# Optimization experiments

Hardware: AMD Instinct MI355X
Metric: run time of the kernel (lower is better)

Reference implementation:

```python
import jax, jax.numpy as jnp
import numpy as np

N = 4096      # sentences in document
K = 32        # clusters (args.k)
D = 256       # input_dim
H = 128       # hidden_dim
P_SAL = 0.5   # args.percent_sal


def setup_inputs() -> dict:
    key = jax.random.key(0)
    ks = jax.random.split(key, 12)
    s = 1.0 / np.sqrt(H)
    inp = {
        "sent_gae_embeds": jax.random.normal(ks[0], (N, D), jnp.float32),
        "labels": jax.random.randint(ks[1], (N,), 0, K),
        # GRU layer 0 (torch gate order r,z,n)
        "W_ih0": jax.random.uniform(ks[2], (3 * H, D), jnp.float32, -s, s),
        "W_hh0": jax.random.uniform(ks[3], (3 * H, H), jnp.float32, -s, s),
        "b_ih0": jax.random.uniform(ks[4], (3 * H,), jnp.float32, -s, s),
        "b_hh0": jax.random.uniform(ks[5], (3 * H,), jnp.float32, -s, s),
        # GRU layer 1
        "W_ih1": jax.random.uniform(ks[6], (3 * H, H), jnp.float32, -s, s),
        "W_hh1": jax.random.uniform(ks[7], (3 * H, H), jnp.float32, -s, s),
        "b_ih1": jax.random.uniform(ks[8], (3 * H,), jnp.float32, -s, s),
        "b_hh1": jax.random.uniform(ks[9], (3 * H,), jnp.float32, -s, s),
        # weight-normed linear: W = g * v / ||v|| (norm over input dim)
        "lin_v": jax.random.normal(ks[10], (1, D + H), jnp.float32) * 0.05,
        "lin_g": jnp.ones((1, 1), jnp.float32),
        "lin_b": jnp.zeros((1,), jnp.float32),
    }
    return inp


def _gru_layer(x, W_ih, W_hh, b_ih, b_hh):
    # x: [T, B, Din] -> outputs [T, B, H]
    xw = jnp.einsum("tbd,gd->tbg", x, W_ih) + b_ih  # precompute input gates

    def step(h, xw_t):
        hw = h @ W_hh.T + b_hh
        r = jax.nn.sigmoid(xw_t[:, :H] + hw[:, :H])
        z = jax.nn.sigmoid(xw_t[:, H:2 * H] + hw[:, H:2 * H])
        n = jnp.tanh(xw_t[:, 2 * H:] + r * hw[:, 2 * H:])
        h_new = (1.0 - z) * n + z * h
        return h_new, h_new

    h0 = jnp.zeros((x.shape[1], H), x.dtype)
    _, outs = jax.lax.scan(step, h0, xw)
    return outs


def reference(sent_gae_embeds, labels, W_ih0, W_hh0, b_ih0, b_hh0,
              W_ih1, W_hh1, b_ih1, b_hh1, lin_v, lin_g, lin_b):
    # --- cluster gather: position of each sentence within its cluster ---
    onehot = jax.nn.one_hot(labels, K, dtype=jnp.int32)          # [N, K]
    pos = jnp.cumsum(onehot, axis=0)[jnp.arange(N), labels] - 1  # [N]
    lengths = onehot.sum(axis=0)                                 # [K]

    # padded per-cluster sequences: [T=N, B=K, D]
    padded = jnp.zeros((N, K, D), sent_gae_embeds.dtype).at[pos, labels].set(sent_gae_embeds)

    # --- 2-layer GRU over each cluster sequence ---
    h1 = _gru_layer(padded, W_ih0, W_hh0, b_ih0, b_hh0)
    h2 = _gru_layer(h1, W_ih1, W_hh1, b_ih1, b_hh1)
    len_c = jnp.maximum(lengths, 1)  # empty cluster -> length-1 zero sequence
    cluster_embeds = h2[len_c - 1, jnp.arange(K)]  # [K, H]

    # --- scatter cluster embeds back onto sentences (sent detached as in torch) ---
    sent_d = jax.lax.stop_gradient(sent_gae_embeds)
    final_embeds = jnp.concatenate([sent_d, cluster_embeds[labels]], axis=-1)  # [N, D+H]

    # weight-normed linear + tanh
    Wn = lin_g * lin_v / jnp.linalg.norm(lin_v, axis=1, keepdims=True)
    scores = jnp.tanh(final_embeds @ Wn.T + lin_b)[:, 0]  # [N]

    # salience: per-cluster segment-sum normalization
    clu_scores = jax.ops.segment_sum(scores, labels, num_segments=K)
    sal_scores = scores / clu_scores[labels]

    # position scores: max(0.5, exp(-(i+1)/n**(1/3)))
    inv = np.float32(1.0 / (N ** (1.0 / 3.0)))
    pos_scores = jnp.maximum(0.5, jnp.exp(-(jnp.arange(N, dtype=jnp.float32) + 1.0) * inv))

    return P_SAL * sal_scores + (1.0 - P_SAL) * pos_scores
```

## Files before the change

kernel.cpp:

```cpp
#include <hip/hip_runtime.h>
#include <cmath>

#define NN 4096
#define KK 32
#define DD 256
#define HH 128
#define G3 384
#define CH 16
#define RH 136

typedef __attribute__((ext_vector_type(8))) _Float16 h8;
typedef __attribute__((ext_vector_type(4))) float f32x4;

__global__ __launch_bounds__(256) void prep_k(
    const int* __restrict__ labels, const float* __restrict__ lin_v,
    const float* __restrict__ lin_g,
    const float* __restrict__ Whh0, const float* __restrict__ Wih1,
    const float* __restrict__ Whh1,
    const float* __restrict__ sent, const float* __restrict__ W_ih0,
    const float* __restrict__ b_ih0,
    int* __restrict__ order, int* __restrict__ len, float* __restrict__ scale,
    _Float16* __restrict__ P, float* __restrict__ xw) {
  const int blk = blockIdx.x;
  const int t = threadIdx.x;
  if (blk < 72) {
    const int gid = blk * 256 + t;
    const int lane = gid & 63;
    const int kt = (gid >> 6) & 3;
    const int nt = (gid >> 8) % 24;
    const int mat = (gid >> 8) / 24;
    const float* W = (mat == 0) ? Whh0 : (mat == 1 ? Wih1 : Whh1);
    const int n = nt * 16 + (lane & 15);
    const int kbase = kt * 32 + (lane >> 4) * 8;
    _Float16* dst = P + (size_t)gid * 8;
#pragma unroll
    for (int j = 0; j < 8; ++j) dst[j] = (_Float16)W[(size_t)n * HH + kbase + j];
    return;
  }
  if (blk < 80) {
    const int wv = t >> 6, lane = t & 63;
    const int c = (blk - 72) * 4 + wv;
    int count = 0;
    for (int base = 0; base < NN; base += 64) {
      const int i = base + lane;
      const bool f = (labels[i] == c);
      const unsigned long long m = __ballot(f);
      if (f) order[c * NN + count + __popcll(m & ((1ull << lane) - 1ull))] = i;
      count += __popcll(m);
    }
    if (lane == 0) len[c] = count;
    return;
  }
  if (blk == 80) {
    if (t < 64) {
      float s = 0.f;
      for (int j = t; j < G3; j += 64) { const float v = lin_v[j]; s += v * v; }
      for (int off = 32; off; off >>= 1) s += __shfl_down(s, off);
      if (t == 0) scale[0] = lin_g[0] / sqrtf(s);
    }
    return;
  }
  __shared__ float Xs[16][132];
  __shared__ float Ws[16][68];
  const int g = blk - 81;
  const int i0 = (g & 31) * 128;
  const int g0 = (g >> 5) * 64;
  const int it = t & 15;
  const int gt = t >> 4;
  float acc[8][4] = {};
  for (int k0 = 0; k0 < DD; k0 += 16) {
#pragma unroll
    for (int l = 0; l < 2; ++l) {
      const int u = t * 2 + l;
      const int r = u >> 2;
      const int cq = u & 3;
      const float4 f = *(const float4*)(sent + (size_t)(i0 + r) * DD + k0 + cq * 4);
      Xs[cq * 4 + 0][r] = f.x; Xs[cq * 4 + 1][r] = f.y;
      Xs[cq * 4 + 2][r] = f.z; Xs[cq * 4 + 3][r] = f.w;
    }
    {
      const int r = t >> 2;
      const int cq = t & 3;
      const float4 f = *(const float4*)(W_ih0 + (size_t)(g0 + r) * DD + k0 + cq * 4);
      Ws[cq * 4 + 0][r] = f.x; Ws[cq * 4 + 1][r] = f.y;
      Ws[cq * 4 + 2][r] = f.z; Ws[cq * 4 + 3][r] = f.w;
    }
    __syncthreads();
#pragma unroll
    for (int k = 0; k < 16; ++k) {
      float a[8], b[4];
#pragma unroll
      for (int x = 0; x < 8; ++x) a[x] = Xs[k][it * 8 + x];
#pragma unroll
      for (int y = 0; y < 4; ++y) b[y] = Ws[k][gt * 4 + y];
#pragma unroll
      for (int x = 0; x < 8; ++x)
#pragma unroll
        for (int y = 0; y < 4; ++y)
          acc[x][y] += a[x] * b[y];
    }
    __syncthreads();
  }
  const float4 bs = *(const float4*)(b_ih0 + g0 + gt * 4);
#pragma unroll
  for (int x = 0; x < 8; ++x) {
    const int gi = i0 + it * 8 + x;
    float4 o;
    o.x = acc[x][0] + bs.x; o.y = acc[x][1] + bs.y;
    o.z = acc[x][2] + bs.z; o.w = acc[x][3] + bs.w;
    *(float4*)(xw + (size_t)gi * G3 + g0 + gt * 4) = o;
  }
}

__global__ __launch_bounds__(768) void gru_fused_k(
    const float* __restrict__ xw0,
    const _Float16* __restrict__ pack,
    const float* __restrict__ b_hh0, const float* __restrict__ b_ih0,
    const float* __restrict__ b_ih1, const float* __restrict__ b_hh1,
    const int* __restrict__ len, const int* __restrict__ order,
    const float* __restrict__ sent,
    const float* __restrict__ lin_v, const float* __restrict__ scale,
    const float* __restrict__ lin_b, float* __restrict__ out) {
  const int c = blockIdx.x;
  const int t = threadIdx.x;
  const int wv = t >> 6, lane = t & 63;
  const int group = wv >> 2;
  const int v = wv & 3;
  h8 B[6][4];
  {
    const _Float16* mp = pack + (size_t)group * (24 * 4 * 64 * 8);
#pragma unroll
    for (int i = 0; i < 6; ++i) {
      const int nt = (i >> 1) * 8 + 2 * v + (i & 1);
#pragma unroll
      for (int kt = 0; kt < 4; ++kt)
        B[i][kt] = *(const h8*)(mp + ((size_t)(nt * 4 + kt) * 64 + lane) * 8);
    }
  }
  const int L = len[c];
  const int Lr = (L > 0) ? L : 1;
  const bool use_bih0 = (L == 0);
  const int u0 = t / 96, f0 = t - u0 * 96;
  const int u1 = (t + 768) / 96, f1 = (t + 768) - u1 * 96;
  __shared__ __align__(16) float xwbuf[2 * CH * G3];
  __shared__ __align__(16) _Float16 ring[16][2 * RH];
  __shared__ __align__(16) _Float16 hp2[2][2][HH];
  __shared__ float xw1buf[2][8][G3];
  __shared__ float ce_s[HH];
  __shared__ float vbuf[G3];
  __shared__ float sc_s[2048];
  __shared__ float sc_red;
  {
    _Float16* rp = &ring[0][0];
    for (int u = t; u < 16 * 2 * RH; u += 768) rp[u] = (_Float16)0.f;
  }
  if (t < HH) {
    hp2[0][0][t] = (_Float16)0.f; hp2[0][1][t] = (_Float16)0.f;
    hp2[1][0][t] = (_Float16)0.f; hp2[1][1][t] = (_Float16)0.f;
  }
  if (!use_bih0) {
    const float4* src = (const float4*)xw0;
    float4* dst = (float4*)xwbuf;
    const int r0 = (u0 < L) ? order[c * NN + u0] : 0;
    const int r1 = (u1 < L) ? order[c * NN + u1] : 0;
    dst[t] = src[(size_t)r0 * 96 + f0];
    dst[t + 768] = src[(size_t)r1 * 96 + f1];
  }
  const int tg = 32 * v + (lane & 31);
  float bhr = 0.f, bhz = 0.f, bhn = 0.f;
  float bir = 0.f, biz = 0.f, bin = 0.f;
  float h = 0.f;
  if (lane < 32) {
    if (group == 0) {
      bhr = b_hh0[tg]; bhz = b_hh0[HH + tg]; bhn = b_hh0[2 * HH + tg];
      if (use_bih0) {
        bir = b_ih0[tg]; biz = b_ih0[HH + tg]; bin = b_ih0[2 * HH + tg];
      }
    } else if (group == 2) {
      bhr = b_hh1[tg]; bhz = b_hh1[HH + tg]; bhn = b_hh1[2 * HH + tg];
      bir = b_ih1[tg]; biz = b_ih1[HH + tg]; bin = b_ih1[2 * HH + tg];
    }
  }
  __syncthreads();
  const int q = lane >> 4;
  const int row = lane & 15;
  const int hs = (row == 0 || row == 4) ? 0 : 1;
  const bool hiacc = ((lane >> 4) & 1) != 0;
  for (int it2 = 0; it2 < Lr + 9; ++it2) {
    const int par = it2 & 1;
    if (!use_bih0 && (it2 & (CH - 1)) == 0 && it2 + CH < Lr) {
      const float4* src = (const float4*)xw0;
      float4* dst = (float4*)(xwbuf + ((((it2 >> 4) + 1) & 1) ? CH * G3 : 0));
      const int p0 = it2 + CH + u0;
      const int p1 = it2 + CH + u1;
      const int r0 = (p0 < L) ? order[c * NN + p0] : 0;
      const int r1 = (p1 < L) ? order[c * NN + p1] : 0;
      dst[t] = src[(size_t)r0 * 96 + f0];
      dst[t + 768] = src[(size_t)r1 * 96 + f1];
    }
    if (group == 0) {
      if (it2 < Lr) {
        float xr = bir, xz = biz, xn = bin;
        if (!use_bih0 && lane < 32) {
          const float* xrow = xwbuf + ((it2 >> 4) & 1) * (CH * G3)
                                    + (it2 & (CH - 1)) * G3;
          xr = xrow[tg]; xz = xrow[HH + tg]; xn = xrow[2 * HH + tg];
        }
        const _Float16* abse = &ring[(it2 - 1) & 15][hs * RH];
        h8 A[4];
#pragma unroll
        for (int kt = 0; kt < 4; ++kt)
          A[kt] = *(const h8*)(abse + kt * 32 + q * 8);
        f32x4 a0[6];
#pragma unroll
        for (int i = 0; i < 6; ++i) {
          f32x4 a = {0.f, 0.f, 0.f, 0.f};
#pragma unroll
          for (int kt = 0; kt < 4; ++kt)
            a = __builtin_amdgcn_mfma_f32_16x16x32_f16(A[kt], B[i][kt], a, 0, 0, 0);
          a0[i] = a;
        }
        if (lane < 32) {
          const float hwrA = a0[0][0] + a0[0][1], hwrB = a0[1][0] + a0[1][1];
          const float hwzA = a0[2][0] + a0[2][1], hwzB = a0[3][0] + a0[3][1];
          const float hwnA = a0[4][0] + a0[4][1], hwnB = a0[5][0] + a0[5][1];
          const float hwr = hiacc ? hwrB : hwrA;
          const float hwz = hiacc ? hwzB : hwzA;
          const float hwn = hiacc ? hwnB : hwnA;
          const float r = 1.f / (1.f + __expf(-(xr + bhr + hwr)));
          const float z = 1.f / (1.f + __expf(-(xz + bhz + hwz)));
          float tgt = xn + r * (bhn + hwn);
          tgt = fminf(fmaxf(tgt, -15.f), 15.f);
          const float e = __expf(2.f * tgt);
          const float n = (e - 1.f) / (e + 1.f);
          h = (1.f - z) * n + z * h;
          const _Float16 hi = (_Float16)h;
          _Float16* rs = &ring[it2 & 15][0];
          rs[tg] = hi;  rs[RH + tg] = (_Float16)(h - (float)hi);
        }
      }
    } else if (group == 1) {
      if (it2 >= 8 && (it2 & 7) == 0 && it2 - 8 < Lr) {
        const int c8 = it2 - 8;
        const int m = lane & 15;
        const int s = m >> 1, half = m & 1;
        const _Float16* abse = &ring[(c8 + s) & 15][half * RH];
        h8 A[4];
#pragma unroll
        for (int kt = 0; kt < 4; ++kt)
          A[kt] = *(const h8*)(abse + kt * 32 + q * 8);
        const int cbuf = (c8 >> 3) & 1;
        float* xo0 = &xw1buf[cbuf][2 * q][0];
        float* xo1 = &xw1buf[cbuf][2 * q + 1][0];
#pragma unroll
        for (int i = 0; i < 6; ++i) {
          f32x4 a = {0.f, 0.f, 0.f, 0.f};
#pragma unroll
          for (int kt = 0; kt < 4; ++kt)
            a = __builtin_amdgcn_mfma_f32_16x16x32_f16(A[kt], B[i][kt], a, 0, 0, 0);
          const int nt = (i >> 1) * 8 + 2 * v + (i & 1);
          const int col = nt * 16 + (lane & 15);
          xo0[col] = a[0] + a[1];
          xo1[col] = a[2] + a[3];
        }
      }
    } else {
      if (it2 >= 9) {
        const int j = it2 - 9;
        float xr = 0.f, xz = 0.f, xn = 0.f;
        if (lane < 32) {
          const float* xi = xw1buf[(j >> 3) & 1][j & 7];
          xr = xi[tg] + bir; xz = xi[HH + tg] + biz; xn = xi[2 * HH + tg] + bin;
        }
        const _Float16* hbase = hp2[par][hs];
        h8 A[4];
#pragma unroll
        for (int kt = 0; kt < 4; ++kt)
          A[kt] = *(const h8*)(hbase + kt * 32 + q * 8);
        f32x4 a1[6];
#pragma unroll
        for (int i = 0; i < 6; ++i) {
          f32x4 a = {0.f, 0.f, 0.f, 0.f};
#pragma unroll
          for (int kt = 0; kt < 4; ++kt)
            a = __builtin_amdgcn_mfma_f32_16x16x32_f16(A[kt], B[i][kt], a, 0, 0, 0);
          a1[i] = a;
        }
        if (lane < 32) {
          const float hwrA = a1[0][0] + a1[0][1], hwrB = a1[1][0] + a1[1][1];
          const float hwzA = a1[2][0] + a1[2][1], hwzB = a1[3][0] + a1[3][1];
          const float hwnA = a1[4][0] + a1[4][1], hwnB = a1[5][0] + a1[5][1];
          const float hwr = hiacc ? hwrB : hwrA;
          const float hwz = hiacc ? hwzB : hwzA;
          const float hwn = hiacc ? hwnB : hwnA;
          const float r = 1.f / (1.f + __expf(-(xr + bhr + hwr)));
          const float z = 1.f / (1.f + __expf(-(xz + bhz + hwz)));
          float tgt = xn + r * (bhn + hwn);
          tgt = fminf(fmaxf(tgt, -15.f), 15.f);
          const float e = __expf(2.f * tgt);
          const float n = (e - 1.f) / (e + 1.f);
          h = (1.f - z) * n + z * h;
          const _Float16 hi = (_Float16)h;
          hp2[par ^ 1][0][tg] = hi;
          hp2[par ^ 1][1][tg] = (_Float16)(h - (float)hi);
        }
      }
    }
    __syncthreads();
  }
  if (L == 0) return;
  if (group == 2 && lane < 32) ce_s[tg] = h;
  if (t < G3) vbuf[t] = lin_v[t];
  __syncthreads();
  if (wv == 0) {
    float cd = ce_s[lane] * vbuf[DD + lane] + ce_s[64 + lane] * vbuf[DD + 64 + lane];
    for (int off = 32; off; off >>= 1) cd += __shfl_down(cd, off);
    if (lane == 0) sc_red = cd;
  }
  __syncthreads();
  const float cedot = sc_red;
  const float sc = scale[0], lb = lin_b[0];
  const int Lc = (L < 2048) ? L : 2048;
  for (int p = wv; p < Lc; p += 12) {
    const int i = order[c * NN + p];
    const float4 a = *(const float4*)(sent + (size_t)i * DD + lane * 4);
    const float4 b = ((const float4*)vbuf)[lane];
    float d = a.x * b.x + a.y * b.y + a.z * b.z + a.w * b.w;
    for (int off = 32; off; off >>= 1) d += __shfl_down(d, off);
    if (lane == 0) sc_s[p] = tanhf(sc * (d + cedot) + lb);
  }
  __syncthreads();
  if (wv == 0) {
    float s = 0.f;
    for (int p = lane; p < Lc; p += 64) s += sc_s[p];
    for (int off = 32; off; off >>= 1) s += __shfl_down(s, off);
    if (lane == 0) sc_red = 1.f / s;
  }
  __syncthreads();
  const float inv = sc_red;
  for (int p = t; p < Lc; p += 768) {
    const int i = order[c * NN + p];
    float ps = __expf(-(float)(i + 1) * 0.0625f);
    ps = fmaxf(0.5f, ps);
    out[i] = 0.5f * (sc_s[p] * inv) + 0.5f * ps;
  }
}

extern "C" void kernel_launch(void* const* d_in, const int* in_sizes, int n_in,
                              void* d_out, int out_size, void* d_ws, size_t ws_size,
                              hipStream_t stream) {
  const float* sent   = (const float*)d_in[0];
  const int*   labels = (const int*)d_in[1];
  const float* W_ih0  = (const float*)d_in[2];
  const float* W_hh0  = (const float*)d_in[3];
  const float* b_ih0  = (const float*)d_in[4];
  const float* b_hh0  = (const float*)d_in[5];
  const float* W_ih1  = (const float*)d_in[6];
  const float* W_hh1  = (const float*)d_in[7];
  const float* b_ih1  = (const float*)d_in[8];
  const float* b_hh1  = (const float*)d_in[9];
  const float* lin_v  = (const float*)d_in[10];
  const float* lin_g  = (const float*)d_in[11];
  const float* lin_b  = (const float*)d_in[12];
  float* out = (float*)d_out;

  char* ws = (char*)d_ws;
  size_t off = 0;
  auto alloc = [&](size_t bytes) -> void* {
    void* p = ws + off;
    off = (off + bytes + 255) & ~(size_t)255;
    return p;
  };
  int*   order  = (int*)  alloc((size_t)KK * NN * sizeof(int));
  int*   len    = (int*)  alloc(KK * sizeof(int));
  float* scale  = (float*)alloc(sizeof(float));
  _Float16* pack = (_Float16*)alloc((size_t)18432 * 8 * sizeof(_Float16));
  float* xw     = (float*)alloc((size_t)NN * G3 * sizeof(float));
  (void)ws_size; (void)in_sizes; (void)n_in; (void)out_size;

  prep_k<<<dim3(273), dim3(256), 0, stream>>>(
      labels, lin_v, lin_g, W_hh0, W_ih1, W_hh1,
      sent, W_ih0, b_ih0, order, len, scale, pack, xw);
  gru_fused_k<<<dim3(KK), dim3(768), 0, stream>>>(
      xw, pack, b_hh0, b_ih0, b_ih1, b_hh1, len, order,
      sent, lin_v, scale, lin_b, out);
}
```

Before: 243.4 us.

## Precompute sentence dot products, prefetch GEMM tiles and xw chunks into registers

Moves the per-sentence dot product with lin_v into extra blocks of the prep kernel, so the GRU kernel's epilogue only reads one float per sentence. The prep GEMM now register-prefetches the next K tile while computing on the current one. The GRU loop splits the xw chunk refill into a global load at phase 6 and an LDS store at phase 14, so the load latency is hidden across recurrence steps. Most __syncthreads become a lighter lgkmcnt wait plus s_barrier. The risks are higher register pressure and the correctness of the weaker barrier, which does not wait on outstanding global loads.

```diff
diff --git a/kernel.cpp b/kernel.cpp
--- a/kernel.cpp
+++ b/kernel.cpp
@@ -11,6 +11,11 @@
 
 typedef __attribute__((ext_vector_type(8))) _Float16 h8;
 typedef __attribute__((ext_vector_type(4))) float f32x4;
+
+__device__ __forceinline__ void bar_lds() {
+  asm volatile("s_waitcnt lgkmcnt(0)" ::: "memory");
+  __builtin_amdgcn_s_barrier();
+}
 
 __global__ __launch_bounds__(256) void prep_k(
     const int* __restrict__ labels, const float* __restrict__ lin_v,
@@ -20,7 +25,8 @@
     const float* __restrict__ sent, const float* __restrict__ W_ih0,
     const float* __restrict__ b_ih0,
     int* __restrict__ order, int* __restrict__ len, float* __restrict__ scale,
-    _Float16* __restrict__ P, float* __restrict__ xw) {
+    _Float16* __restrict__ P, float* __restrict__ xw,
+    float* __restrict__ sdot) {
   const int blk = blockIdx.x;
   const int t = threadIdx.x;
   if (blk < 72) {
@@ -60,6 +66,20 @@
     }
     return;
   }
+  if (blk >= 273) {
+    const int b = blk - 273;
+    const int wv = t >> 6, lane = t & 63;
+    const float4 vv = *(const float4*)(lin_v + lane * 4);
+    const int r0 = b * 64 + wv * 16;
+    for (int rr = 0; rr < 16; ++rr) {
+      const int r = r0 + rr;
+      const float4 a = *(const float4*)(sent + (size_t)r * DD + lane * 4);
+      float d = a.x * vv.x + a.y * vv.y + a.z * vv.z + a.w * vv.w;
+      for (int off = 32; off; off >>= 1) d += __shfl_down(d, off);
+      if (lane == 0) sdot[r] = d;
+    }
+    return;
+  }
   __shared__ float Xs[16][132];
   __shared__ float Ws[16][68];
   const int g = blk - 81;
@@ -67,25 +87,29 @@
   const int g0 = (g >> 5) * 64;
   const int it = t & 15;
   const int gt = t >> 4;
+  const int u0 = t * 2, u1 = t * 2 + 1;
+  const int ra0 = u0 >> 2, ca0 = u0 & 3;
+  const int ra1 = u1 >> 2, ca1 = u1 & 3;
+  const int rw_ = t >> 2, cw_ = t & 3;
   float acc[8][4] = {};
+  float4 x0, x1, w0;
+  x0 = *(const float4*)(sent + (size_t)(i0 + ra0) * DD + ca0 * 4);
+  x1 = *(const float4*)(sent + (size_t)(i0 + ra1) * DD + ca1 * 4);
+  w0 = *(const float4*)(W_ih0 + (size_t)(g0 + rw_) * DD + cw_ * 4);
   for (int k0 = 0; k0 < DD; k0 += 16) {
-#pragma unroll
-    for (int l = 0; l < 2; ++l) {
-      const int u = t * 2 + l;
-      const int r = u >> 2;
-      const int cq = u & 3;
-      const float4 f = *(const float4*)(sent + (size_t)(i0 + r) * DD + k0 + cq * 4);
-      Xs[cq * 4 + 0][r] = f.x; Xs[cq * 4 + 1][r] = f.y;
-      Xs[cq * 4 + 2][r] = f.z; Xs[cq * 4 + 3][r] = f.w;
-    }
-    {
-      const int r = t >> 2;
-      const int cq = t & 3;
-      const float4 f = *(const float4*)(W_ih0 + (size_t)(g0 + r) * DD + k0 + cq * 4);
-      Ws[cq * 4 + 0][r] = f.x; Ws[cq * 4 + 1][r] = f.y;
-      Ws[cq * 4 + 2][r] = f.z; Ws[cq * 4 + 3][r] = f.w;
-    }
-    __syncthreads();
+    Xs[ca0 * 4 + 0][ra0] = x0.x; Xs[ca0 * 4 + 1][ra0] = x0.y;
+    Xs[ca0 * 4 + 2][ra0] = x0.z; Xs[ca0 * 4 + 3][ra0] = x0.w;
+    Xs[ca1 * 4 + 0][ra1] = x1.x; Xs[ca1 * 4 + 1][ra1] = x1.y;
+    Xs[ca1 * 4 + 2][ra1] = x1.z; Xs[ca1 * 4 + 3][ra1] = x1.w;
+    Ws[cw_ * 4 + 0][rw_] = w0.x; Ws[cw_ * 4 + 1][rw_] = w0.y;
+    Ws[cw_ * 4 + 2][rw_] = w0.z; Ws[cw_ * 4 + 3][rw_] = w0.w;
+    bar_lds();
+    if (k0 + 16 < DD) {
+      const int kn = k0 + 16;
+      x0 = *(const float4*)(sent + (size_t)(i0 + ra0) * DD + kn + ca0 * 4);
+      x1 = *(const float4*)(sent + (size_t)(i0 + ra1) * DD + kn + ca1 * 4);
+      w0 = *(const float4*)(W_ih0 + (size_t)(g0 + rw_) * DD + kn + cw_ * 4);
+    }
 #pragma unroll
     for (int k = 0; k < 16; ++k) {
       float a[8], b[4];
@@ -99,7 +123,7 @@
         for (int y = 0; y < 4; ++y)
           acc[x][y] += a[x] * b[y];
     }
-    __syncthreads();
+    bar_lds();
   }
   const float4 bs = *(const float4*)(b_ih0 + g0 + gt * 4);
 #pragma unroll
@@ -118,7 +142,7 @@
     const float* __restrict__ b_hh0, const float* __restrict__ b_ih0,
     const float* __restrict__ b_ih1, const float* __restrict__ b_hh1,
     const int* __restrict__ len, const int* __restrict__ order,
-    const float* __restrict__ sent,
+    const float* __restrict__ sdot,
     const float* __restrict__ lin_v, const float* __restrict__ scale,
     const float* __restrict__ lin_b, float* __restrict__ out) {
   const int c = blockIdx.x;
@@ -142,12 +166,13 @@
   const bool use_bih0 = (L == 0);
   const int u0 = t / 96, f0 = t - u0 * 96;
   const int u1 = (t + 768) / 96, f1 = (t + 768) - u1 * 96;
+  const float4* const xsrc = (const float4*)xw0;
   __shared__ __align__(16) float xwbuf[2 * CH * G3];
   __shared__ __align__(16) _Float16 ring[16][2 * RH];
   __shared__ __align__(16) _Float16 hp2[2][2][HH];
   __shared__ float xw1buf[2][8][G3];
   __shared__ float ce_s[HH];
-  __shared__ float vbuf[G3];
+  __shared__ float vbuf[HH];
   __shared__ float sc_s[2048];
   __shared__ float sc_red;
   {
@@ -159,12 +184,11 @@
     hp2[1][0][t] = (_Float16)0.f; hp2[1][1][t] = (_Float16)0.f;
   }
   if (!use_bih0) {
-    const float4* src = (const float4*)xw0;
     float4* dst = (float4*)xwbuf;
     const int r0 = (u0 < L) ? order[c * NN + u0] : 0;
     const int r1 = (u1 < L) ? order[c * NN + u1] : 0;
-    dst[t] = src[(size_t)r0 * 96 + f0];
-    dst[t + 768] = src[(size_t)r1 * 96 + f1];
+    dst[t] = xsrc[(size_t)r0 * 96 + f0];
+    dst[t + 768] = xsrc[(size_t)r1 * 96 + f1];
   }
   const int tg = 32 * v + (lane & 31);
   float bhr = 0.f, bhz = 0.f, bhn = 0.f;
@@ -186,17 +210,30 @@
   const int row = lane & 15;
   const int hs = (row == 0 || row == 4) ? 0 : 1;
   const bool hiacc = ((lane >> 4) & 1) != 0;
+  float4 pf0 = {0.f, 0.f, 0.f, 0.f}, pf1 = {0.f, 0.f, 0.f, 0.f};
+  bool pfv = false;
   for (int it2 = 0; it2 < Lr + 9; ++it2) {
     const int par = it2 & 1;
-    if (!use_bih0 && (it2 & (CH - 1)) == 0 && it2 + CH < Lr) {
-      const float4* src = (const float4*)xw0;
-      float4* dst = (float4*)(xwbuf + ((((it2 >> 4) + 1) & 1) ? CH * G3 : 0));
-      const int p0 = it2 + CH + u0;
-      const int p1 = it2 + CH + u1;
-      const int r0 = (p0 < L) ? order[c * NN + p0] : 0;
-      const int r1 = (p1 < L) ? order[c * NN + p1] : 0;
-      dst[t] = src[(size_t)r0 * 96 + f0];
-      dst[t + 768] = src[(size_t)r1 * 96 + f1];
+    const int ph = it2 & (CH - 1);
+    if (!use_bih0) {
+      if (ph == 6) {
+        const int s = (it2 & ~(CH - 1)) + CH;
+        if (s < Lr) {
+          const int p0 = s + u0;
+          const int p1 = s + u1;
+          const int r0 = (p0 < L) ? order[c * NN + p0] : 0;
+          const int r1 = (p1 < L) ? order[c * NN + p1] : 0;
+          pf0 = xsrc[(size_t)r0 * 96 + f0];
+          pf1 = xsrc[(size_t)r1 * 96 + f1];
+          pfv = true;
+        }
+      } else if (ph == 14 && pfv) {
+        const int s = (it2 & ~(CH - 1)) + CH;
+        float4* dst = (float4*)(xwbuf + (((s >> 4) & 1) ? CH * G3 : 0));
+        dst[t] = pf0;
+        dst[t + 768] = pf1;
+        pfv = false;
+      }
     }
     if (group == 0) {
       if (it2 < Lr) {
@@ -306,14 +343,14 @@
         }
       }
     }
-    __syncthreads();
+    bar_lds();
   }
   if (L == 0) return;
   if (group == 2 && lane < 32) ce_s[tg] = h;
-  if (t < G3) vbuf[t] = lin_v[t];
+  if (t < HH) vbuf[t] = lin_v[DD + t];
   __syncthreads();
   if (wv == 0) {
-    float cd = ce_s[lane] * vbuf[DD + lane] + ce_s[64 + lane] * vbuf[DD + 64 + lane];
+    float cd = ce_s[lane] * vbuf[lane] + ce_s[64 + lane] * vbuf[64 + lane];
     for (int off = 32; off; off >>= 1) cd += __shfl_down(cd, off);
     if (lane == 0) sc_red = cd;
   }
@@ -321,13 +358,9 @@
   const float cedot = sc_red;
   const float sc = scale[0], lb = lin_b[0];
   const int Lc = (L < 2048) ? L : 2048;
-  for (int p = wv; p < Lc; p += 12) {
+  for (int p = t; p < Lc; p += 768) {
     const int i = order[c * NN + p];
-    const float4 a = *(const float4*)(sent + (size_t)i * DD + lane * 4);
-    const float4 b = ((const float4*)vbuf)[lane];
-    float d = a.x * b.x + a.y * b.y + a.z * b.z + a.w * b.w;
-    for (int off = 32; off; off >>= 1) d += __shfl_down(d, off);
-    if (lane == 0) sc_s[p] = tanhf(sc * (d + cedot) + lb);
+    sc_s[p] = tanhf(sc * (sdot[i] + cedot) + lb);
   }
   __syncthreads();
   if (wv == 0) {
@@ -376,12 +409,13 @@
   float* scale  = (float*)alloc(sizeof(float));
   _Float16* pack = (_Float16*)alloc((size_t)18432 * 8 * sizeof(_Float16));
   float* xw     = (float*)alloc((size_t)NN * G3 * sizeof(float));
+  float* sdot   = (float*)alloc((size_t)NN * sizeof(float));
   (void)ws_size; (void)in_sizes; (void)n_in; (void)out_size;
 
-  prep_k<<<dim3(273), dim3(256), 0, stream>>>(
+  prep_k<<<dim3(337), dim3(256), 0, stream>>>(
       labels, lin_v, lin_g, W_hh0, W_ih1, W_hh1,
-      sent, W_ih0, b_ih0, order, len, scale, pack, xw);
+      sent, W_ih0, b_ih0, order, len, scale, pack, xw, sdot);
   gru_fused_k<<<dim3(KK), dim3(768), 0, stream>>>(
       xw, pack, b_hh0, b_ih0, b_ih1, b_hh1, len, order,
-      sent, lin_v, scale, lin_b, out);
+      sdot, lin_v, scale, lin_b, out);
 }
```

Result: faster. 235.7 us, median of 2 (-3.2%).
